# Kernel optimization log

Hardware: AMD Instinct MI355X
Metric: run time of the kernel (lower is better)

Reference implementation:

```python
import jax, jax.numpy as jnp
import numpy as np

N_NODES = 50000
N_EDGES = 800000
IN_DIM, HID_DIM, OUT_DIM = 512, 64, 40
DROPOUT_P = 0.5


def _gcn_conv(h, src, dst, deg_inv_sqrt, W, b, n_nodes):
    # PyG GCNConv (normalize=True, add_self_loops=True):
    #   h' = h @ W; out[dst] += d^-1/2[src] * d^-1/2[dst] * h'[src]; out += b
    # src/dst already include self-loops; deg_inv_sqrt precomputed from them.
    ht = h @ W                                            # [N, F_out]
    norm = deg_inv_sqrt[src] * deg_inv_sqrt[dst]          # [E+N]
    msg = ht[src] * norm[:, None]                         # [E+N, F_out]
    out = jax.ops.segment_sum(msg, dst, num_segments=n_nodes)
    return out + b


def setup_inputs() -> dict:
    key = jax.random.key(0)
    k1, k2, k3, k4 = jax.random.split(key, 4)
    x = jax.random.normal(k1, (N_NODES, IN_DIM), dtype=jnp.float32)
    edge_index = jax.random.randint(k2, (2, N_EDGES), 0, N_NODES, dtype=jnp.int32)
    W1 = jax.random.normal(k3, (IN_DIM, HID_DIM), dtype=jnp.float32) / np.sqrt(IN_DIM)
    b1 = jnp.zeros((HID_DIM,), dtype=jnp.float32)
    W2 = jax.random.normal(k4, (HID_DIM, OUT_DIM), dtype=jnp.float32) / np.sqrt(HID_DIM)
    b2 = jnp.zeros((OUT_DIM,), dtype=jnp.float32)
    return {"x": x, "edge_index": edge_index, "W1": W1, "b1": b1, "W2": W2, "b2": b2}


def reference(x, edge_index, W1, b1, W2, b2):
    n = x.shape[0]
    loop = jnp.arange(n, dtype=edge_index.dtype)
    src = jnp.concatenate([edge_index[0], loop])          # add self-loops
    dst = jnp.concatenate([edge_index[1], loop])
    deg = jax.ops.segment_sum(jnp.ones_like(dst, dtype=x.dtype), dst, num_segments=n)
    deg_inv_sqrt = jnp.where(deg > 0, jax.lax.rsqrt(deg), 0.0)

    h = _gcn_conv(x, src, dst, deg_inv_sqrt, W1, b1, n)
    h = jax.nn.relu(h)
    # dropout (training=True) with a fixed key for determinism
    keep = jax.random.bernoulli(jax.random.key(42), 1.0 - DROPOUT_P, h.shape)
    h = jnp.where(keep, h / (1.0 - DROPOUT_P), 0.0)
    h = _gcn_conv(h, src, dst, deg_inv_sqrt, W2, b2, n)
    return jax.nn.log_softmax(h, axis=1)
```

## Files before the change

### kernel.cpp

```cpp
#include <hip/hip_runtime.h>
#include <math.h>
#include <float.h>

#define N_NODES 50000
#define N_EDGES 800000
#define IN_DIM  512
#define HID_DIM 64
#define OUT_DIM 40
#define GEMM1_BLOCKS 782
#define FILL_BLOCKS 1568
#define NODES_PER_GRP 6250
#define BCAP 96
#define AGG_Q 1563
#define AGG_BLOCKS (8 * AGG_Q)
#define GF_BLOCKS 2350

typedef __attribute__((ext_vector_type(8))) short bf16x8;
typedef __attribute__((ext_vector_type(4))) float f32x4;

#define GLOAD_LDS(SRC, DST)                                                   \
  __builtin_amdgcn_global_load_lds(                                           \
      (const __attribute__((address_space(1))) void*)(SRC),                   \
      (__attribute__((address_space(3))) void*)(DST), 16, 0, 0)

__device__ __forceinline__ unsigned rotl32(unsigned v, int n) {
  return (v << n) | (v >> (32 - n));
}

__device__ __forceinline__ void threefry2x32_0_42(unsigned x0, unsigned x1,
                                                  unsigned &o0, unsigned &o1) {
  const unsigned ks0 = 0u;
  const unsigned ks1 = 42u;
  const unsigned ks2 = 0u ^ 42u ^ 0x1BD11BDAu;
  x0 += ks0; x1 += ks1;
  x0 += x1; x1 = rotl32(x1, 13); x1 ^= x0;
  x0 += x1; x1 = rotl32(x1, 15); x1 ^= x0;
  x0 += x1; x1 = rotl32(x1, 26); x1 ^= x0;
  x0 += x1; x1 = rotl32(x1,  6); x1 ^= x0;
  x0 += ks1; x1 += ks2 + 1u;
  x0 += x1; x1 = rotl32(x1, 17); x1 ^= x0;
  x0 += x1; x1 = rotl32(x1, 29); x1 ^= x0;
  x0 += x1; x1 = rotl32(x1, 16); x1 ^= x0;
  x0 += x1; x1 = rotl32(x1, 24); x1 ^= x0;
  x0 += ks2; x1 += ks0 + 2u;
  x0 += x1; x1 = rotl32(x1, 13); x1 ^= x0;
  x0 += x1; x1 = rotl32(x1, 15); x1 ^= x0;
  x0 += x1; x1 = rotl32(x1, 26); x1 ^= x0;
  x0 += x1; x1 = rotl32(x1,  6); x1 ^= x0;
  x0 += ks0; x1 += ks1 + 3u;
  x0 += x1; x1 = rotl32(x1, 17); x1 ^= x0;
  x0 += x1; x1 = rotl32(x1, 29); x1 ^= x0;
  x0 += x1; x1 = rotl32(x1, 16); x1 ^= x0;
  x0 += x1; x1 = rotl32(x1, 24); x1 ^= x0;
  x0 += ks1; x1 += ks2 + 4u;
  x0 += x1; x1 = rotl32(x1, 13); x1 ^= x0;
  x0 += x1; x1 = rotl32(x1, 15); x1 ^= x0;
  x0 += x1; x1 = rotl32(x1, 26); x1 ^= x0;
  x0 += x1; x1 = rotl32(x1,  6); x1 ^= x0;
  x0 += ks2; x1 += ks0 + 5u;
  o0 = x0; o1 = x1;
}

__device__ __forceinline__ unsigned short f2bf(float f) {
  unsigned u = __float_as_uint(f);
  unsigned r = u + 0x7FFFu + ((u >> 16) & 1u);
  return (unsigned short)(r >> 16);
}

__global__ void k_init(const float* __restrict__ W1, const float* __restrict__ W2,
                       unsigned short* __restrict__ Wb1, float* __restrict__ w2t,
                       int* __restrict__ cnt) {
  int i = blockIdx.x * 256 + threadIdx.x;
  if (i < N_NODES) cnt[i] = 0;
  if (i < IN_DIM * HID_DIM) {
    int j = i & 7;
    int lane = (i >> 3) & 63;
    int cg = (i >> 9) & 3;
    int kb = i >> 11;
    int k = kb * 32 + ((lane >> 4) << 3) + j;
    int c = cg * 16 + (lane & 15);
    Wb1[i] = f2bf(W1[k * HID_DIM + c]);
  }
  if (i < HID_DIM * OUT_DIM) {
    int j = i >> 6;
    int k = i & 63;
    w2t[i] = W2[k * OUT_DIM + j];
  }
}

__global__ __launch_bounds__(512) void k_gemm1_fill(
    const int* __restrict__ ei, int* __restrict__ cnt,
    unsigned short* __restrict__ elist2,
    const float* __restrict__ x, const unsigned short* __restrict__ Wb1,
    unsigned short* __restrict__ ht1b) {
  __shared__ unsigned char sxa[2][16384];

  const int b = blockIdx.x;
  const int q = b / 3;
  const int r = b - 3 * q;
  const bool is_gemm = (r == 0) && (q < GEMM1_BLOCKS);

  if (!is_gemm) {
    int fb = (b < 3 * GEMM1_BLOCKS) ? (2 * q + r - 1) : (1564 + (b - 2346));
    if (fb >= FILL_BLOCKS) return;
    const int grp = fb & 7;
    const int ord = fb >> 3;
    const int lo = grp * NODES_PER_GRP;
    const int hi = lo + NODES_PER_GRP;
    const int ebase = ord * 512 + threadIdx.x;
    int dv[8];
#pragma unroll
    for (int i = 0; i < 8; ++i) {
      int e = ebase + i * (196 * 512);
      dv[i] = (e < N_EDGES) ? ei[N_EDGES + e] : -1;
    }
#pragma unroll
    for (int i = 0; i < 8; ++i) {
      if (dv[i] >= lo && dv[i] < hi) {
        int s = ei[ebase + i * (196 * 512)];
        int slot = atomicAdd(&cnt[dv[i]], 1);
        if (slot < BCAP) elist2[dv[i] * BCAP + slot] = (unsigned short)s;
      }
    }
    return;
  }

  const int tid = threadIdx.x;
  const int lane = tid & 63;
  const int wave = tid >> 6;
  const int brow = q * 64;

  f32x4 acc[2];
  acc[0] = (f32x4){0.f, 0.f, 0.f, 0.f};
  acc[1] = (f32x4){0.f, 0.f, 0.f, 0.f};

  const bf16x8* __restrict__ Wv = (const bf16x8*)Wb1;

  int srow[2], soff[2];
#pragma unroll
  for (int i = 0; i < 2; ++i) {
    int p = wave * 2048 + i * 1024 + lane * 16;
    int row = p >> 8;
    int bb = p & 255;
    int gr2 = brow + row;
    if (gr2 >= N_NODES) gr2 = N_NODES - 1;
    srow[i] = gr2;
    soff[i] = bb ^ ((row & 7) << 4);
  }

#define ISSUE(B, KC)                                                          \
  {                                                                           \
    _Pragma("unroll")                                                         \
    for (int i = 0; i < 2; ++i) {                                             \
      const char* src = (const char*)(x + (size_t)srow[i] * IN_DIM +          \
                                      (KC) * 64) + soff[i];                   \
      GLOAD_LDS(src, &sxa[B][wave * 2048 + i * 1024]);                        \
    }                                                                         \
  }

  ISSUE(0, 0)
  __syncthreads();

  const int arow = 16 * (wave & 3) + (lane & 15);
  const int rsw = (arow & 7) << 4;
  const int kbyte = (lane >> 4) << 5;
  const int cgb = 2 * (wave >> 2);

  int buf = 0;
  for (int kc = 0; kc < 8; ++kc) {
    if (kc < 7) ISSUE(buf ^ 1, kc + 1)
#pragma unroll
    for (int ks = 0; ks < 2; ++ks) {
      int lin = arow * 256 + ks * 128 + kbyte;
      float4 fa = *(const float4*)(&sxa[buf][lin ^ rsw]);
      float4 fb4 = *(const float4*)(&sxa[buf][(lin + 16) ^ rsw]);
      union { unsigned short u[8]; bf16x8 v; } pk;
      pk.u[0] = f2bf(fa.x); pk.u[1] = f2bf(fa.y);
      pk.u[2] = f2bf(fa.z); pk.u[3] = f2bf(fa.w);
      pk.u[4] = f2bf(fb4.x); pk.u[5] = f2bf(fb4.y);
      pk.u[6] = f2bf(fb4.z); pk.u[7] = f2bf(fb4.w);
      int kb = kc * 2 + ks;
#pragma unroll
      for (int c = 0; c < 2; ++c) {
        bf16x8 bw = Wv[(kb * 4 + cgb + c) * 64 + lane];
        acc[c] = __builtin_amdgcn_mfma_f32_16x16x32_bf16(pk.v, bw, acc[c], 0, 0, 0);
      }
    }
    __syncthreads();
    buf ^= 1;
  }
#undef ISSUE

#pragma unroll
  for (int p = 0; p < 4; ++p) {
    int grow = brow + 16 * (wave & 3) + ((lane >> 4) << 2) + p;
    if (grow < N_NODES) {
#pragma unroll
      for (int c = 0; c < 2; ++c) {
        ht1b[(size_t)grow * HID_DIM + (cgb + c) * 16 + (lane & 15)] =
            f2bf(acc[c][p]);
      }
    }
  }
}

__global__ __launch_bounds__(256) void k_agg1g2(const int* __restrict__ cnt,
                                                const unsigned short* __restrict__ elist2,
                                                const unsigned short* __restrict__ ht1b,
                                                const float* __restrict__ b1,
                                                const float* __restrict__ w2t,
                                                unsigned short* __restrict__ ht2b) {
  const int wave = threadIdx.x >> 6;
  const int lane = threadIdx.x & 63;
  const int dl = (blockIdx.x >> 3) * 4 + wave;
  if (dl >= NODES_PER_GRP) return;
  const int d = (blockIdx.x & 7) * NODES_PER_GRP + dl;
  const int g = lane >> 3;
  const int fh = lane & 7;

  unsigned t0, t1;
  threefry2x32_0_42(0u, (unsigned)d * 64u + (unsigned)lane, t0, t1);
  unsigned long long keep = __ballot(!((t0 ^ t1) & 0x80000000u));

  int cn = cnt[d];
  if (cn > BCAP) cn = BCAP;
  const unsigned short* __restrict__ bucket = elist2 + d * BCAP;
  float4 a0 = {0.f, 0.f, 0.f, 0.f};
  float4 a1 = {0.f, 0.f, 0.f, 0.f};
#pragma unroll 2
  for (int j = g; j < cn; j += 8) {
    int s = bucket[j];
    float ds = rsqrtf((float)cnt[s] + 1.0f);
    const uint2* __restrict__ p = (const uint2*)(ht1b + (size_t)s * HID_DIM);
    uint2 q0 = p[fh];
    uint2 q1 = p[fh + 8];
    a0.x += __uint_as_float(q0.x << 16) * ds;
    a0.y += __uint_as_float(q0.x & 0xFFFF0000u) * ds;
    a0.z += __uint_as_float(q0.y << 16) * ds;
    a0.w += __uint_as_float(q0.y & 0xFFFF0000u) * ds;
    a1.x += __uint_as_float(q1.x << 16) * ds;
    a1.y += __uint_as_float(q1.x & 0xFFFF0000u) * ds;
    a1.z += __uint_as_float(q1.y << 16) * ds;
    a1.w += __uint_as_float(q1.y & 0xFFFF0000u) * ds;
  }
#pragma unroll
  for (int m = 32; m >= 8; m >>= 1) {
    a0.x += __shfl_xor(a0.x, m); a0.y += __shfl_xor(a0.y, m);
    a0.z += __shfl_xor(a0.z, m); a0.w += __shfl_xor(a0.w, m);
    a1.x += __shfl_xor(a1.x, m); a1.y += __shfl_xor(a1.y, m);
    a1.z += __shfl_xor(a1.z, m); a1.w += __shfl_xor(a1.w, m);
  }

  float dd = rsqrtf((float)cn + 1.0f);
  {
    const uint2* __restrict__ ps = (const uint2*)(ht1b + (size_t)d * HID_DIM);
    uint2 s0 = ps[fh];
    uint2 s1 = ps[fh + 8];
    a0.x += __uint_as_float(s0.x << 16) * dd;
    a0.y += __uint_as_float(s0.x & 0xFFFF0000u) * dd;
    a0.z += __uint_as_float(s0.y << 16) * dd;
    a0.w += __uint_as_float(s0.y & 0xFFFF0000u) * dd;
    a1.x += __uint_as_float(s1.x << 16) * dd;
    a1.y += __uint_as_float(s1.x & 0xFFFF0000u) * dd;
    a1.z += __uint_as_float(s1.y << 16) * dd;
    a1.w += __uint_as_float(s1.y & 0xFFFF0000u) * dd;
  }
  float4 bb0 = *(const float4*)(b1 + fh * 4);
  float4 bb1 = *(const float4*)(b1 + fh * 4 + 32);
  int f0 = fh * 4;
  float4 v0, v1;
  v0.x = fmaxf(a0.x * dd + bb0.x, 0.f) * (((keep >> (f0 + 0)) & 1) ? 2.f : 0.f);
  v0.y = fmaxf(a0.y * dd + bb0.y, 0.f) * (((keep >> (f0 + 1)) & 1) ? 2.f : 0.f);
  v0.z = fmaxf(a0.z * dd + bb0.z, 0.f) * (((keep >> (f0 + 2)) & 1) ? 2.f : 0.f);
  v0.w = fmaxf(a0.w * dd + bb0.w, 0.f) * (((keep >> (f0 + 3)) & 1) ? 2.f : 0.f);
  v1.x = fmaxf(a1.x * dd + bb1.x, 0.f) * (((keep >> (f0 + 32)) & 1) ? 2.f : 0.f);
  v1.y = fmaxf(a1.y * dd + bb1.y, 0.f) * (((keep >> (f0 + 33)) & 1) ? 2.f : 0.f);
  v1.z = fmaxf(a1.z * dd + bb1.z, 0.f) * (((keep >> (f0 + 34)) & 1) ? 2.f : 0.f);
  v1.w = fmaxf(a1.w * dd + bb1.w, 0.f) * (((keep >> (f0 + 35)) & 1) ? 2.f : 0.f);

  const int jb = g * 5;
  float part[5];
#pragma unroll
  for (int c = 0; c < 5; ++c) {
    const float* __restrict__ wr = w2t + (jb + c) * 64;
    float4 wA = *(const float4*)(wr + f0);
    float4 wB = *(const float4*)(wr + 32 + f0);
    part[c] = v0.x * wA.x + v0.y * wA.y + v0.z * wA.z + v0.w * wA.w +
              v1.x * wB.x + v1.y * wB.y + v1.z * wB.z + v1.w * wB.w;
  }
#pragma unroll
  for (int c = 0; c < 5; ++c) {
    part[c] += __shfl_xor(part[c], 1);
    part[c] += __shfl_xor(part[c], 2);
    part[c] += __shfl_xor(part[c], 4);
  }
  if (fh == 0) {
#pragma unroll
    for (int c = 0; c < 5; ++c)
      ht2b[(size_t)d * OUT_DIM + jb + c] = f2bf(part[c] * dd);
  }
}

__global__ __launch_bounds__(256) void k_agg2(const int* __restrict__ cnt,
                                              const unsigned short* __restrict__ elist2,
                                              const unsigned short* __restrict__ ht2b,
                                              const float* __restrict__ b2,
                                              float* __restrict__ out) {
  const int wave = threadIdx.x >> 6;
  const int lane = threadIdx.x & 63;
  const int dl = (blockIdx.x >> 3) * 4 + wave;
  if (dl >= NODES_PER_GRP) return;
  const int d = (blockIdx.x & 7) * NODES_PER_GRP + dl;
  const int g = lane >> 3;
  const int fh = lane & 7;
  const bool extra = fh < 2;

  int cn = cnt[d];
  if (cn > BCAP) cn = BCAP;
  const unsigned short* __restrict__ bucket = elist2 + d * BCAP;
  float4 a0 = {0.f, 0.f, 0.f, 0.f};
  float4 a1 = {0.f, 0.f, 0.f, 0.f};
#pragma unroll 2
  for (int j = g; j < cn; j += 8) {
    int s = bucket[j];
    const uint2* __restrict__ p = (const uint2*)(ht2b + (size_t)s * OUT_DIM);
    uint2 q0 = p[fh];
    a0.x += __uint_as_float(q0.x << 16);
    a0.y += __uint_as_float(q0.x & 0xFFFF0000u);
    a0.z += __uint_as_float(q0.y << 16);
    a0.w += __uint_as_float(q0.y & 0xFFFF0000u);
    if (extra) {
      uint2 q1 = p[8 + fh];
      a1.x += __uint_as_float(q1.x << 16);
      a1.y += __uint_as_float(q1.x & 0xFFFF0000u);
      a1.z += __uint_as_float(q1.y << 16);
      a1.w += __uint_as_float(q1.y & 0xFFFF0000u);
    }
  }
#pragma unroll
  for (int m = 32; m >= 8; m >>= 1) {
    a0.x += __shfl_xor(a0.x, m); a0.y += __shfl_xor(a0.y, m);
    a0.z += __shfl_xor(a0.z, m); a0.w += __shfl_xor(a0.w, m);
    a1.x += __shfl_xor(a1.x, m); a1.y += __shfl_xor(a1.y, m);
    a1.z += __shfl_xor(a1.z, m); a1.w += __shfl_xor(a1.w, m);
  }

  {
    const uint2* __restrict__ ps = (const uint2*)(ht2b + (size_t)d * OUT_DIM);
    uint2 s0 = ps[fh];
    a0.x += __uint_as_float(s0.x << 16);
    a0.y += __uint_as_float(s0.x & 0xFFFF0000u);
    a0.z += __uint_as_float(s0.y << 16);
    a0.w += __uint_as_float(s0.y & 0xFFFF0000u);
    if (extra) {
      uint2 s1 = ps[8 + fh];
      a1.x += __uint_as_float(s1.x << 16);
      a1.y += __uint_as_float(s1.x & 0xFFFF0000u);
      a1.z += __uint_as_float(s1.y << 16);
      a1.w += __uint_as_float(s1.y & 0xFFFF0000u);
    }
  }

  float dd = rsqrtf((float)cn + 1.0f);
  float4 bb0 = *(const float4*)(b2 + fh * 4);
  float4 v0, v1;
  v0.x = a0.x * dd + bb0.x;
  v0.y = a0.y * dd + bb0.y;
  v0.z = a0.z * dd + bb0.z;
  v0.w = a0.w * dd + bb0.w;
  float mm = fmaxf(fmaxf(v0.x, v0.y), fmaxf(v0.z, v0.w));
  if (extra) {
    float4 bb1 = *(const float4*)(b2 + 32 + fh * 4);
    v1.x = a1.x * dd + bb1.x;
    v1.y = a1.y * dd + bb1.y;
    v1.z = a1.z * dd + bb1.z;
    v1.w = a1.w * dd + bb1.w;
    mm = fmaxf(mm, fmaxf(fmaxf(v1.x, v1.y), fmaxf(v1.z, v1.w)));
  }
  mm = fmaxf(mm, __shfl_xor(mm, 1));
  mm = fmaxf(mm, __shfl_xor(mm, 2));
  mm = fmaxf(mm, __shfl_xor(mm, 4));
  float e = expf(v0.x - mm) + expf(v0.y - mm) + expf(v0.z - mm) + expf(v0.w - mm);
  if (extra)
    e += expf(v1.x - mm) + expf(v1.y - mm) + expf(v1.z - mm) + expf(v1.w - mm);
  e += __shfl_xor(e, 1);
  e += __shfl_xor(e, 2);
  e += __shfl_xor(e, 4);
  float ls = logf(e) + mm;

  if (g == 0) {
    float4 r;
    r.x = v0.x - ls; r.y = v0.y - ls; r.z = v0.z - ls; r.w = v0.w - ls;
    *(float4*)(out + (size_t)d * OUT_DIM + fh * 4) = r;
    if (extra) {
      float4 r1;
      r1.x = v1.x - ls; r1.y = v1.y - ls; r1.z = v1.z - ls; r1.w = v1.w - ls;
      *(float4*)(out + (size_t)d * OUT_DIM + 32 + fh * 4) = r1;
    }
  }
}

extern "C" void kernel_launch(void* const* d_in, const int* in_sizes, int n_in,
                              void* d_out, int out_size, void* d_ws, size_t ws_size,
                              hipStream_t stream) {
  const float* x  = (const float*)d_in[0];
  const int*   ei = (const int*)  d_in[1];
  const float* W1 = (const float*)d_in[2];
  const float* b1 = (const float*)d_in[3];
  const float* W2 = (const float*)d_in[4];
  const float* b2 = (const float*)d_in[5];
  float* out = (float*)d_out;
  float* ws  = (float*)d_ws;

  unsigned short* ht1b = (unsigned short*)ws;
  unsigned short* ht2b = (unsigned short*)(ws + 1600000);
  unsigned short* Wb1 = (unsigned short*)(ws + 2600000);
  float* w2t  = ws + 2620000;
  int* cnt    = (int*)(ws + 2630000);
  unsigned short* elist2 = (unsigned short*)(ws + 2681200);

  k_init<<<196, 256, 0, stream>>>(W1, W2, Wb1, w2t, cnt);
  k_gemm1_fill<<<GF_BLOCKS, 512, 0, stream>>>(ei, cnt, elist2, x, Wb1, ht1b);
  k_agg1g2<<<AGG_BLOCKS, 256, 0, stream>>>(cnt, elist2, ht1b, b1, w2t, ht2b);
  k_agg2<<<AGG_BLOCKS, 256, 0, stream>>>(cnt, elist2, ht2b, b2, out);
}
```

Before: 125.8 us.

## Replace LDS-staged GEMM1 with direct global loads and 128-row tiles

The first-layer GEMM no longer stages x through double-buffered LDS via global_load_lds with barriers. Each wave now reads its own 16 rows directly from global memory and computes all four 16-column output groups, so a block covers 128 rows instead of 64. The GEMM/fill block interleaving is rebalanced to one GEMM block per five, which halves the GEMM block count. The aim is to remove LDS traffic and sync overhead; the risk is less coalesced global loads, since each lane reads 32-byte chunks strided by the row, and less latency hiding without the prefetch.

After: 142.3 us. +13.2%, slower.

```diff
diff --git a/kernel.cpp b/kernel.cpp
--- a/kernel.cpp
+++ b/kernel.cpp
@@ -7,21 +7,16 @@
 #define IN_DIM  512
 #define HID_DIM 64
 #define OUT_DIM 40
-#define GEMM1_BLOCKS 782
+#define G1_BLOCKS 391
 #define FILL_BLOCKS 1568
 #define NODES_PER_GRP 6250
 #define BCAP 96
 #define AGG_Q 1563
 #define AGG_BLOCKS (8 * AGG_Q)
-#define GF_BLOCKS 2350
+#define GF_BLOCKS 1959
 
 typedef __attribute__((ext_vector_type(8))) short bf16x8;
 typedef __attribute__((ext_vector_type(4))) float f32x4;
-
-#define GLOAD_LDS(SRC, DST)                                                   \
-  __builtin_amdgcn_global_load_lds(                                           \
-      (const __attribute__((address_space(1))) void*)(SRC),                   \
-      (__attribute__((address_space(3))) void*)(DST), 16, 0, 0)
 
 __device__ __forceinline__ unsigned rotl32(unsigned v, int n) {
   return (v << n) | (v >> (32 - n));
@@ -93,15 +88,13 @@
     unsigned short* __restrict__ elist2,
     const float* __restrict__ x, const unsigned short* __restrict__ Wb1,
     unsigned short* __restrict__ ht1b) {
-  __shared__ unsigned char sxa[2][16384];
-
   const int b = blockIdx.x;
-  const int q = b / 3;
-  const int r = b - 3 * q;
-  const bool is_gemm = (r == 0) && (q < GEMM1_BLOCKS);
+  const int q = b / 5;
+  const int r = b - 5 * q;
+  const bool is_gemm = (r == 0) && (q < G1_BLOCKS);
 
   if (!is_gemm) {
-    int fb = (b < 3 * GEMM1_BLOCKS) ? (2 * q + r - 1) : (1564 + (b - 2346));
+    int fb = (b < 5 * G1_BLOCKS) ? (4 * q + r - 1) : (1564 + (b - 1955));
     if (fb >= FILL_BLOCKS) return;
     const int grp = fb & 7;
     const int ord = fb >> 3;
@@ -125,80 +118,43 @@
     return;
   }
 
-  const int tid = threadIdx.x;
-  const int lane = tid & 63;
-  const int wave = tid >> 6;
-  const int brow = q * 64;
-
-  f32x4 acc[2];
-  acc[0] = (f32x4){0.f, 0.f, 0.f, 0.f};
-  acc[1] = (f32x4){0.f, 0.f, 0.f, 0.f};
+  const int lane = threadIdx.x & 63;
+  const int wave = threadIdx.x >> 6;
+  const int brow = q * 128;
+
+  int arow = brow + 16 * wave + (lane & 15);
+  if (arow >= N_NODES) arow = N_NODES - 1;
+  const float* __restrict__ xrow = x + (size_t)arow * IN_DIM + ((lane >> 4) << 3);
+
+  f32x4 acc[4];
+#pragma unroll
+  for (int c = 0; c < 4; ++c) acc[c] = (f32x4){0.f, 0.f, 0.f, 0.f};
 
   const bf16x8* __restrict__ Wv = (const bf16x8*)Wb1;
 
-  int srow[2], soff[2];
-#pragma unroll
-  for (int i = 0; i < 2; ++i) {
-    int p = wave * 2048 + i * 1024 + lane * 16;
-    int row = p >> 8;
-    int bb = p & 255;
-    int gr2 = brow + row;
-    if (gr2 >= N_NODES) gr2 = N_NODES - 1;
-    srow[i] = gr2;
-    soff[i] = bb ^ ((row & 7) << 4);
-  }
-
-#define ISSUE(B, KC)                                                          \
-  {                                                                           \
-    _Pragma("unroll")                                                         \
-    for (int i = 0; i < 2; ++i) {                                             \
-      const char* src = (const char*)(x + (size_t)srow[i] * IN_DIM +          \
-                                      (KC) * 64) + soff[i];                   \
-      GLOAD_LDS(src, &sxa[B][wave * 2048 + i * 1024]);                        \
-    }                                                                         \
-  }
-
-  ISSUE(0, 0)
-  __syncthreads();
-
-  const int arow = 16 * (wave & 3) + (lane & 15);
-  const int rsw = (arow & 7) << 4;
-  const int kbyte = (lane >> 4) << 5;
-  const int cgb = 2 * (wave >> 2);
-
-  int buf = 0;
-  for (int kc = 0; kc < 8; ++kc) {
-    if (kc < 7) ISSUE(buf ^ 1, kc + 1)
-#pragma unroll
-    for (int ks = 0; ks < 2; ++ks) {
-      int lin = arow * 256 + ks * 128 + kbyte;
-      float4 fa = *(const float4*)(&sxa[buf][lin ^ rsw]);
-      float4 fb4 = *(const float4*)(&sxa[buf][(lin + 16) ^ rsw]);
-      union { unsigned short u[8]; bf16x8 v; } pk;
-      pk.u[0] = f2bf(fa.x); pk.u[1] = f2bf(fa.y);
-      pk.u[2] = f2bf(fa.z); pk.u[3] = f2bf(fa.w);
-      pk.u[4] = f2bf(fb4.x); pk.u[5] = f2bf(fb4.y);
-      pk.u[6] = f2bf(fb4.z); pk.u[7] = f2bf(fb4.w);
-      int kb = kc * 2 + ks;
-#pragma unroll
-      for (int c = 0; c < 2; ++c) {
-        bf16x8 bw = Wv[(kb * 4 + cgb + c) * 64 + lane];
-        acc[c] = __builtin_amdgcn_mfma_f32_16x16x32_bf16(pk.v, bw, acc[c], 0, 0, 0);
-      }
-    }
-    __syncthreads();
-    buf ^= 1;
-  }
-#undef ISSUE
+#pragma unroll 4
+  for (int kb = 0; kb < 16; ++kb) {
+    float4 fa = *(const float4*)(xrow + kb * 32);
+    float4 fb4 = *(const float4*)(xrow + kb * 32 + 4);
+    union { unsigned short u[8]; bf16x8 v; } pk;
+    pk.u[0] = f2bf(fa.x); pk.u[1] = f2bf(fa.y);
+    pk.u[2] = f2bf(fa.z); pk.u[3] = f2bf(fa.w);
+    pk.u[4] = f2bf(fb4.x); pk.u[5] = f2bf(fb4.y);
+    pk.u[6] = f2bf(fb4.z); pk.u[7] = f2bf(fb4.w);
+#pragma unroll
+    for (int c = 0; c < 4; ++c) {
+      bf16x8 bw = Wv[(kb * 4 + c) * 64 + lane];
+      acc[c] = __builtin_amdgcn_mfma_f32_16x16x32_bf16(pk.v, bw, acc[c], 0, 0, 0);
+    }
+  }
 
 #pragma unroll
   for (int p = 0; p < 4; ++p) {
-    int grow = brow + 16 * (wave & 3) + ((lane >> 4) << 2) + p;
+    int grow = brow + 16 * wave + ((lane >> 4) << 2) + p;
     if (grow < N_NODES) {
 #pragma unroll
-      for (int c = 0; c < 2; ++c) {
-        ht1b[(size_t)grow * HID_DIM + (cgb + c) * 16 + (lane & 15)] =
-            f2bf(acc[c][p]);
+      for (int c = 0; c < 4; ++c) {
+        ht1b[(size_t)grow * HID_DIM + c * 16 + (lane & 15)] = f2bf(acc[c][p]);
       }
     }
   }
```
